# Performance work log

Hardware: AMD Instinct MI355X
Metric: run time of the kernel (lower is better)

## Reference

```python
import jax, jax.numpy as jnp
import numpy as np

D_MODEL = 256
NUM_HEADS = 4
D_HEAD = D_MODEL // NUM_HEADS
LN_EPS = 1e-5
NEG_INF = -1e9


def setup_inputs() -> dict:
    key = jax.random.key(0)
    ks = jax.random.split(key, 8)
    B, N = 4, 2048
    s = 1.0 / np.sqrt(D_MODEL)
    return {
        "x": jax.random.normal(ks[0], (B, N, D_MODEL), dtype=jnp.float32),
        "Wq": jax.random.normal(ks[1], (D_MODEL, D_MODEL), dtype=jnp.float32) * s,
        "Wk": jax.random.normal(ks[2], (D_MODEL, D_MODEL), dtype=jnp.float32) * s,
        "Wv": jax.random.normal(ks[3], (D_MODEL, D_MODEL), dtype=jnp.float32) * s,
        "Wo": jax.random.normal(ks[4], (D_MODEL, D_MODEL), dtype=jnp.float32) * s,
        "bo": jnp.zeros((D_MODEL,), dtype=jnp.float32),
        "gamma": jnp.ones((D_MODEL,), dtype=jnp.float32),
        "beta": jnp.zeros((D_MODEL,), dtype=jnp.float32),
        "k_neighbors": 8,
    }


def build_knn_adj(x, k):
    # x: [B, N, D]; returns symmetric 0/1 adjacency [B, N, N]
    B, N, _ = x.shape
    xn = x / jnp.maximum(jnp.linalg.norm(x, axis=-1, keepdims=True), 1e-12)
    sim = jnp.einsum('bnd,bmd->bnm', xn, xn)  # [B, N, N]
    _, idx = jax.lax.top_k(sim, k + 1)        # [B, N, k+1]
    b = jnp.arange(B)[:, None, None]
    r = jnp.arange(N)[None, :, None]
    adj = jnp.zeros((B, N, N), dtype=jnp.float32).at[b, r, idx].add(1.0)
    adj = jnp.maximum(adj, jnp.swapaxes(adj, 1, 2))
    return adj


def layer_norm(x, gamma, beta):
    mu = jnp.mean(x, axis=-1, keepdims=True)
    var = jnp.mean(jnp.square(x - mu), axis=-1, keepdims=True)
    return (x - mu) * jax.lax.rsqrt(var + LN_EPS) * gamma + beta


def reference(x, Wq, Wk, Wv, Wo, bo, gamma, beta, k_neighbors):
    B, N, D = x.shape
    adj = build_knn_adj(x, k_neighbors)  # [B, N, N]

    def split_heads(t):  # [B, N, D] -> [B, H, N, d]
        return jnp.transpose(t.reshape(B, N, NUM_HEADS, D_HEAD), (0, 2, 1, 3))

    q = split_heads(x @ Wq)
    k = split_heads(x @ Wk)
    v = split_heads(x @ Wv)

    scores = jnp.einsum('bhnd,bhmd->bhnm', q, k) / jnp.sqrt(jnp.float32(D_HEAD))
    scores = jnp.where(adj[:, None, :, :] > 0, scores, NEG_INF)
    attn = jax.nn.softmax(scores, axis=-1)  # dropout is identity at inference
    out = jnp.einsum('bhnm,bhmd->bhnd', attn, v)
    out = jnp.transpose(out, (0, 2, 1, 3)).reshape(B, N, D)
    out = out @ Wo + bo
    return layer_norm(x + out, gamma, beta)
```

## Files before the change

### kernel.cpp

```cpp
#include <hip/hip_runtime.h>
#include <hip/hip_bf16.h>
#include <math.h>

#define BATCH 4
#define N 2048
#define D 256
#define NH 4
#define DH 64
#define TOPK 9
#define NEG_BIG -1e30f

typedef __bf16 bf16;
typedef __bf16 bf16x4 __attribute__((ext_vector_type(4)));
typedef __bf16 bf16x8 __attribute__((ext_vector_type(8)));
typedef float f32x4 __attribute__((ext_vector_type(4)));

#define PK3(a,b,c) ((a) | ((b) << 2) | ((c) << 4))
#define PK6(a,b,c,d,e,f) ((a) | ((b) << 2) | ((c) << 4) | ((d) << 6) | ((e) << 8) | ((f) << 10))

#define WAITVM(Nc) __builtin_amdgcn_s_waitcnt((((Nc) & 0xf)) | (7u << 4) | (0xfu << 8) | ((((unsigned)(Nc)) >> 4) << 14))

__device__ __forceinline__ void async_cp16(const bf16* g, const bf16* l) {
  __builtin_amdgcn_global_load_lds(
      (const __attribute__((address_space(1))) void*)(uintptr_t)g,
      (__attribute__((address_space(3))) void*)(uintptr_t)l, 16, 0, 0);
}

__global__ __launch_bounds__(64) void prep_kernel(const float* __restrict__ x,
                                                  const float* __restrict__ Wq,
                                                  const float* __restrict__ Wk,
                                                  const float* __restrict__ Wv,
                                                  const float* __restrict__ Wo,
                                                  bf16* __restrict__ XsN,
                                                  bf16* __restrict__ Wt,
                                                  float* __restrict__ norms,
                                                  uint4* __restrict__ mask4) {
  int blk = blockIdx.x;
  int lane = threadIdx.x;
  if (blk < 8192) {
    float4 v = *(const float4*)(x + (size_t)blk * D + lane * 4);
    float ss = v.x * v.x + v.y * v.y + v.z * v.z + v.w * v.w;
    for (int off = 32; off; off >>= 1) ss += __shfl_down(ss, off);
    ss = __shfl(ss, 0);
    float nrm = fmaxf(sqrtf(ss), 1e-12f);
    if (lane == 0) norms[blk] = nrm;
    float sc = 1.0f / nrm;
    float xs[4] = {v.x * sc, v.y * sc, v.z * sc, v.w * sc};
    bf16* o = XsN + (size_t)blk * 512 + lane * 4;
#pragma unroll
    for (int j = 0; j < 4; ++j) {
      float xv = xs[j];
      bf16 h = (bf16)xv;
      o[j] = h;
      o[256 + j] = (bf16)(xv - (float)h);
    }
  } else if (blk < 9216) {
    int jj = blk - 8192;
    const float* W = (jj < 256) ? Wq : (jj < 512) ? Wk : (jj < 768) ? Wv : Wo;
    int j = jj & 255;
    bf16* dst = Wt + (size_t)jj * 512;
    for (int k = lane; k < 256; k += 64) {
      float w = W[(size_t)k * D + j];
      bf16 h = (bf16)w;
      dst[k] = h;
      dst[256 + k] = (bf16)(w - (float)h);
    }
  } else {
    int base = (blk - 9216) * 1024 + lane;
#pragma unroll
    for (int t = 0; t < 16; ++t)
      mask4[base + t * 64] = make_uint4(0, 0, 0, 0);
  }
}

__device__ __forceinline__ void gemm_core128x256(bf16* As, bf16* Bs,
                                                 const bf16* __restrict__ Ab,
                                                 const bf16* __restrict__ Bb,
                                                 void* __restrict__ Cvoid,
                                                 int ldc, int nsteps,
                                                 int amap, int bmap,
                                                 int row0, int col0,
                                                 int outmode, bool mirror,
                                                 const float* __restrict__ rowscale) {
  int tid = threadIdx.x;
  int lane = tid & 63;
  int wv = tid >> 6;
  int wm = (wv >> 1) * 64;
  int wn = (wv & 1) * 128;
  int fr = lane & 15;
  int G = lane >> 4;

  f32x4 acc[4][8] = {};

  auto issue = [&](int st, int buf) {
    int ch = st >> 3;
    int aoff = (((amap >> (ch * 2)) & 3) << 8) | ((st & 7) << 5);
    int boff = (((bmap >> (ch * 2)) & 3) << 8) | ((st & 7) << 5);
#pragma unroll
    for (int q = 0; q < 2; ++q) {
      int s = q * 256 + tid;
      int r = s >> 2, sl = s & 3;
      async_cp16(Ab + (size_t)r * 512 + ((sl ^ ((r >> 1) & 3)) << 3) + aoff,
                 &As[buf * 4096 + s * 8]);
    }
#pragma unroll
    for (int q = 0; q < 4; ++q) {
      int s = q * 256 + tid;
      int r = s >> 2, sl = s & 3;
      async_cp16(Bb + (size_t)r * 512 + ((sl ^ ((r >> 1) & 3)) << 3) + boff,
                 &Bs[buf * 8192 + s * 8]);
    }
  };

  issue(0, 0);
  for (int st = 0; st < nsteps; ++st) {
    int buf = st & 1;
    if (st + 1 < nsteps) {
      issue(st + 1, buf ^ 1);
      WAITVM(6);
    } else {
      WAITVM(0);
    }
    __builtin_amdgcn_s_barrier();
    bf16x8 af[4], bfr[8];
#pragma unroll
    for (int mi = 0; mi < 4; ++mi) {
      int r = wm + mi * 16 + fr;
      af[mi] = *(const bf16x8*)&As[buf * 4096 + r * 32 + ((G ^ ((r >> 1) & 3)) << 3)];
    }
#pragma unroll
    for (int nj = 0; nj < 8; ++nj) {
      int r = wn + nj * 16 + fr;
      bfr[nj] = *(const bf16x8*)&Bs[buf * 8192 + r * 32 + ((G ^ ((r >> 1) & 3)) << 3)];
    }
    __builtin_amdgcn_s_setprio(1);
#pragma unroll
    for (int mi = 0; mi < 4; ++mi)
#pragma unroll
      for (int nj = 0; nj < 8; ++nj)
        acc[mi][nj] = __builtin_amdgcn_mfma_f32_16x16x32_bf16(af[mi], bfr[nj], acc[mi][nj], 0, 0, 0);
    __builtin_amdgcn_s_setprio(0);
    __builtin_amdgcn_s_barrier();
  }

  int er = (lane >> 4) * 4;
  int ec = lane & 15;
#pragma unroll
  for (int mi = 0; mi < 4; ++mi) {
    int rb = row0 + wm + mi * 16 + er;
    float scl[4] = {1.f, 1.f, 1.f, 1.f};
    if (rowscale) {
      float4 s4 = *(const float4*)(rowscale + rb);
      scl[0] = s4.x; scl[1] = s4.y; scl[2] = s4.z; scl[3] = s4.w;
    }
#pragma unroll
    for (int nj = 0; nj < 8; ++nj) {
      int cb = col0 + wn + nj * 16 + ec;
      if (outmode == 1) {
        float* Cb = (float*)Cvoid;
#pragma unroll
        for (int reg = 0; reg < 4; ++reg)
          __builtin_nontemporal_store(acc[mi][nj][reg],
                                      &Cb[(size_t)(rb + reg) * ldc + cb]);
        if (mirror) {
          __builtin_nontemporal_store(acc[mi][nj],
                                      (f32x4*)&Cb[(size_t)cb * ldc + rb]);
        }
      } else {
        bf16* Cb = (bf16*)Cvoid;
#pragma unroll
        for (int reg = 0; reg < 4; ++reg)
          Cb[(size_t)(rb + reg) * ldc + cb] = (bf16)(acc[mi][nj][reg] * scl[reg]);
      }
    }
  }
}

__global__ __launch_bounds__(256, 2) void gemm_fused128x256_kernel(
    const bf16* __restrict__ XsN, float* __restrict__ sim,
    int amap_s, int bmap_s,
    const bf16* __restrict__ Wt, bf16* __restrict__ qkv,
    int amap_q, int bmap_q, const float* __restrict__ norms) {
  __shared__ bf16 As[2 * 128 * 32];
  __shared__ bf16 Bs[2 * 256 * 32];
  int g = blockIdx.x;
  if (g < 288) {
    int xcd = g & 7;
    int z = xcd >> 1;
    int t = (xcd & 1) * 36 + (g >> 3);
    int half = t & 1;
    int u = t >> 1;
    int by = 0;
    while (u >= 8 - by) { u -= 8 - by; ++by; }
    int bx = by + u;
    int row0 = by * 256 + half * 128;
    int col0 = bx * 256;
    gemm_core128x256(As, Bs,
                     XsN + (size_t)z * N * 512 + (size_t)row0 * 512,
                     XsN + (size_t)z * N * 512 + (size_t)col0 * 512,
                     sim + (size_t)z * N * N,
                     N, 24, amap_s, bmap_s, row0, col0,
                     1, bx != by, nullptr);
  } else {
    int t = g - 288;
    int xcd = t & 7;
    int slot = t >> 3;
    int z = xcd >> 1;
    int by = z * 16 + (xcd & 1) * 8 + slot / 3;
    int bx = slot % 3;
    gemm_core128x256(As, Bs,
                     XsN + (size_t)by * 128 * 512,
                     Wt + (size_t)bx * 256 * 512,
                     qkv, 768, 16, amap_q, bmap_q,
                     by * 128, bx * 256, 2, false, norms);
  }
}

__device__ __forceinline__ void gemm_core(bf16* As, bf16* Bs,
                                          const bf16* __restrict__ Ab,
                                          const bf16* __restrict__ Bb,
                                          void* __restrict__ Cvoid,
                                          int lda, int ldb, int ldc,
                                          int nsteps, int amap, int bmap,
                                          int row0, int col0,
                                          int outmode, bool mirror,
                                          const float* __restrict__ rowscale) {
  int tid = threadIdx.x;
  int lane = tid & 63;
  int wv = tid >> 6;
  int wm = (wv >> 1) * 64;
  int wn = (wv & 1) * 64;

  int rbase = tid >> 2;
  int gperm = (tid & 3) ^ ((rbase >> 1) & 3);
  const bf16* ga0 = Ab + (size_t)rbase * lda + gperm * 8;
  const bf16* gb0 = Bb + (size_t)rbase * ldb + gperm * 8;
  int ldsoff = tid * 8;

  int fr = lane & 15;
  int G = lane >> 4;

  f32x4 acc[4][4] = {};

  auto issue = [&](int st, int buf) {
    int ch = st >> 3;
    int aoff = (((amap >> (ch * 2)) & 3) << 8) | ((st & 7) << 5);
    int boff = (((bmap >> (ch * 2)) & 3) << 8) | ((st & 7) << 5);
#pragma unroll
    for (int q = 0; q < 2; ++q)
      async_cp16(ga0 + (size_t)q * 64 * lda + aoff, &As[buf * 4096 + ldsoff + q * 2048]);
#pragma unroll
    for (int q = 0; q < 2; ++q)
      async_cp16(gb0 + (size_t)q * 64 * ldb + boff, &Bs[buf * 4096 + ldsoff + q * 2048]);
  };

  issue(0, 0);
  for (int st = 0; st < nsteps; ++st) {
    int buf = st & 1;
    if (st + 1 < nsteps) {
      issue(st + 1, buf ^ 1);
      WAITVM(4);
    } else {
      WAITVM(0);
    }
    __builtin_amdgcn_s_barrier();
    bf16x8 af[4], bfr[4];
#pragma unroll
    for (int mi = 0; mi < 4; ++mi) {
      int r = wm + mi * 16 + fr;
      af[mi] = *(const bf16x8*)&As[buf * 4096 + r * 32 + ((G ^ ((r >> 1) & 3)) << 3)];
    }
#pragma unroll
    for (int nj = 0; nj < 4; ++nj) {
      int r = wn + nj * 16 + fr;
      bfr[nj] = *(const bf16x8*)&Bs[buf * 4096 + r * 32 + ((G ^ ((r >> 1) & 3)) << 3)];
    }
#pragma unroll
    for (int mi = 0; mi < 4; ++mi)
#pragma unroll
      for (int nj = 0; nj < 4; ++nj)
        acc[mi][nj] = __builtin_amdgcn_mfma_f32_16x16x32_bf16(af[mi], bfr[nj], acc[mi][nj], 0, 0, 0);
    __builtin_amdgcn_s_barrier();
  }

  int er = (lane >> 4) * 4;
  int ec = lane & 15;
#pragma unroll
  for (int mi = 0; mi < 4; ++mi) {
    int rb = row0 + wm + mi * 16 + er;
    float scl[4] = {1.f, 1.f, 1.f, 1.f};
    if (rowscale) {
      float4 s4 = *(const float4*)(rowscale + rb);
      scl[0] = s4.x; scl[1] = s4.y; scl[2] = s4.z; scl[3] = s4.w;
    }
#pragma unroll
    for (int nj = 0; nj < 4; ++nj) {
      int cb = col0 + wn + nj * 16 + ec;
      if (outmode == 1) {
        float* Cb = (float*)Cvoid;
#pragma unroll
        for (int reg = 0; reg < 4; ++reg)
          __builtin_nontemporal_store(acc[mi][nj][reg],
                                      &Cb[(size_t)(rb + reg) * ldc + cb]);
        if (mirror) {
#pragma unroll
          for (int reg = 0; reg < 4; ++reg)
            __builtin_nontemporal_store(acc[mi][nj][reg],
                                        &Cb[(size_t)cb * ldc + rb + reg]);
        }
      } else {
        bf16* Cb = (bf16*)Cvoid;
#pragma unroll
        for (int reg = 0; reg < 4; ++reg)
          Cb[(size_t)(rb + reg) * ldc + cb] = (bf16)(acc[mi][nj][reg] * scl[reg]);
      }
    }
  }
}

__global__ __launch_bounds__(256, 4) void gemm_sim_kernel(const bf16* __restrict__ XsN,
                                                          float* __restrict__ sim,
                                                          int amap, int bmap) {
  __shared__ bf16 As[2 * 128 * 32];
  __shared__ bf16 Bs[2 * 128 * 32];
  int g = blockIdx.x;
  int xcd = g & 7;
  int slot = g >> 3;
  int z = xcd >> 1;
  int t = (xcd & 1) * 68 + slot;
  int by = 0;
  while (t >= 16 - by) { t -= 16 - by; ++by; }
  int bx = by + t;
  gemm_core(As, Bs,
            XsN + (size_t)z * N * 512 + (size_t)by * 128 * 512,
            XsN + (size_t)z * N * 512 + (size_t)bx * 128 * 512,
            sim + (size_t)z * N * N,
            512, 512, N, 24, amap, bmap, by * 128, bx * 128,
            1, bx != by, nullptr);
}

__global__ __launch_bounds__(256, 4) void gemm_qkv_kernel(const bf16* __restrict__ XsN,
                                                          const bf16* __restrict__ Wt,
                                                          bf16* __restrict__ qkv,
                                                          int amap, int bmap,
                                                          const float* __restrict__ norms) {
  __shared__ bf16 As[2 * 128 * 32];
  __shared__ bf16 Bs[2 * 128 * 32];
  gemm_core(As, Bs,
            XsN + (size_t)blockIdx.y * 128 * 512,
            Wt + (size_t)blockIdx.x * 128 * 512,
            qkv, 512, 512, 768, 16, amap, bmap,
            blockIdx.y * 128, blockIdx.x * 128, 2, false, norms);
}

__global__ __launch_bounds__(64) void topk_adj_kernel(const float* __restrict__ sim,
                                                      unsigned* __restrict__ mask) {
  int row = blockIdx.x;
  int lane = threadIdx.x;
  int b = row >> 11, r = row & 2047;
  const float* srow = sim + (size_t)row * N;
  float v[32];
#pragma unroll
  for (int it = 0; it < 8; ++it) {
    float4 q = *(const float4*)(srow + it * 256 + lane * 4);
    v[it * 4 + 0] = q.x; v[it * 4 + 1] = q.y;
    v[it * 4 + 2] = q.z; v[it * 4 + 3] = q.w;
  }
  unsigned removed = 0;
  for (int rs = 0; rs < TOPK; ++rs) {
    float m = -3e38f;
    int mi = 0;
#pragma unroll
    for (int i = 0; i < 32; ++i) {
      float vv = ((removed >> i) & 1u) ? -3e38f : v[i];
      if (vv > m) { m = vv; mi = i; }
    }
    int gidx = ((mi >> 2) << 8) + lane * 4 + (mi & 3);
    for (int off = 32; off; off >>= 1) {
      float om = __shfl_down(m, off);
      int og = __shfl_down(gidx, off);
      if (om > m || (om == m && og < gidx)) { m = om; gidx = og; }
    }
    gidx = __shfl(gidx, 0);
    if (((gidx >> 2) & 63) == lane)
      removed |= 1u << (((gidx >> 8) << 2) | (gidx & 3));
    if (lane == 0) {
      atomicOr(&mask[(size_t)row * 64 + (gidx >> 5)], 1u << (gidx & 31));
      atomicOr(&mask[(((size_t)b << 11) + gidx) * 64 + (r >> 5)], 1u << (r & 31));
    }
  }
}

__global__ __launch_bounds__(256) void attn_kernel(const bf16* __restrict__ qkv,
                                                   const unsigned* __restrict__ mask,
                                                   bf16* __restrict__ aos) {
  __shared__ float sq[4][256];
  __shared__ unsigned short nbr[4][2048];
  __shared__ int s_nn[4];
  int wv = threadIdx.x >> 6;
  int lane = threadIdx.x & 63;
  int hl = lane >> 4;
  int g = blockIdx.x;
  int xcd = g & 7;
  int b = xcd >> 1;
  int tile = (xcd & 1) * 256 + (g >> 3);
  int bn = b * N + tile * 4 + wv;
  if (lane == 0) s_nn[wv] = 0;
  {
    bf16x4 qv = *(const bf16x4*)(qkv + (size_t)bn * 768 + lane * 4);
#pragma unroll
    for (int j = 0; j < 4; ++j) sq[wv][lane * 4 + j] = (float)qv[j];
  }
  __syncthreads();
  unsigned bits = mask[(size_t)bn * (N / 32) + lane];
  while (bits) {
    int bit = __ffs(bits) - 1;
    bits &= bits - 1;
    int p = atomicAdd(&s_nn[wv], 1);
    nbr[wv][p] = (unsigned short)(lane * 32 + bit);
  }
  __syncthreads();
  int nn = s_nn[wv];
  const bf16* base = qkv + (size_t)b * N * 768;
  float acc2[4] = {0.f, 0.f, 0.f, 0.f};

  auto score4 = [&](int j, float* s) {
    const bf16* kr = base + (size_t)j * 768 + 256;
#pragma unroll
    for (int h = 0; h < 4; ++h) {
      float a = 0.f;
#pragma unroll
      for (int c = 0; c < DH; c += 8) {
        bf16x8 kk = *(const bf16x8*)(kr + h * DH + c);
#pragma unroll
        for (int t = 0; t < 8; ++t) a += sq[wv][h * DH + c + t] * (float)kk[t];
      }
      s[h] = a * 0.125f;
    }
  };

  if (nn <= 64) {
    float s[4] = {NEG_BIG, NEG_BIG, NEG_BIG, NEG_BIG};
    if (lane < nn) score4(nbr[wv][lane], s);
    float w[4], l[4];
#pragma unroll
    for (int h = 0; h < 4; ++h) {
      float m = s[h];
      for (int off = 32; off; off >>= 1) m = fmaxf(m, __shfl_down(m, off));
      m = __shfl(m, 0);
      float e = (lane < nn) ? __expf(s[h] - m) : 0.f;
      float ls = e;
      for (int off = 32; off; off >>= 1) ls += __shfl_down(ls, off);
      l[h] = __shfl(ls, 0);
      w[h] = e;
    }
    auto pickw = [&](int ii) {
      float a0 = __shfl(w[0], ii), a1 = __shfl(w[1], ii);
      float a2 = __shfl(w[2], ii), a3 = __shfl(w[3], ii);
      return hl == 0 ? a0 : (hl == 1 ? a1 : (hl == 2 ? a2 : a3));
    };
    int i = 0;
    for (; i + 4 <= nn; i += 4) {
      int j0 = nbr[wv][i + 0], j1 = nbr[wv][i + 1];
      int j2 = nbr[wv][i + 2], j3 = nbr[wv][i + 3];
      bf16x4 v0 = *(const bf16x4*)(base + (size_t)j0 * 768 + 512 + lane * 4);
      bf16x4 v1 = *(const bf16x4*)(base + (size_t)j1 * 768 + 512 + lane * 4);
      bf16x4 v2 = *(const bf16x4*)(base + (size_t)j2 * 768 + 512 + lane * 4);
      bf16x4 v3 = *(const bf16x4*)(base + (size_t)j3 * 768 + 512 + lane * 4);
      float w0 = pickw(i + 0), w1 = pickw(i + 1);
      float w2 = pickw(i + 2), w3 = pickw(i + 3);
#pragma unroll
      for (int t = 0; t < 4; ++t)
        acc2[t] += w0 * (float)v0[t] + w1 * (float)v1[t] +
                   w2 * (float)v2[t] + w3 * (float)v3[t];
    }
    for (; i < nn; ++i) {
      bf16x4 v0 = *(const bf16x4*)(base + (size_t)nbr[wv][i] * 768 + 512 + lane * 4);
      float w0 = pickw(i);
#pragma unroll
      for (int t = 0; t < 4; ++t) acc2[t] += w0 * (float)v0[t];
    }
    float ldiv = hl == 0 ? l[0] : (hl == 1 ? l[1] : (hl == 2 ? l[2] : l[3]));
#pragma unroll
    for (int t = 0; t < 4; ++t) acc2[t] /= ldiv;
  } else {
    float m[4] = {NEG_BIG, NEG_BIG, NEG_BIG, NEG_BIG};
    for (int i0 = 0; i0 < nn; i0 += 64) {
      float s[4] = {NEG_BIG, NEG_BIG, NEG_BIG, NEG_BIG};
      if (i0 + lane < nn) score4(nbr[wv][i0 + lane], s);
#pragma unroll
      for (int h = 0; h < 4; ++h) m[h] = fmaxf(m[h], s[h]);
    }
#pragma unroll
    for (int h = 0; h < 4; ++h) {
      for (int off = 32; off; off >>= 1) m[h] = fmaxf(m[h], __shfl_down(m[h], off));
      m[h] = __shfl(m[h], 0);
    }
    float l[4] = {0.f, 0.f, 0.f, 0.f};
    for (int i0 = 0; i0 < nn; i0 += 64) {
      float s[4] = {NEG_BIG, NEG_BIG, NEG_BIG, NEG_BIG};
      if (i0 + lane < nn) score4(nbr[wv][i0 + lane], s);
      float e[4];
#pragma unroll
      for (int h = 0; h < 4; ++h) {
        e[h] = (i0 + lane < nn) ? __expf(s[h] - m[h]) : 0.f;
        float ls = e[h];
        for (int off = 32; off; off >>= 1) ls += __shfl_down(ls, off);
        l[h] += __shfl(ls, 0);
      }
      auto picke = [&](int ii) {
        float a0 = __shfl(e[0], ii), a1 = __shfl(e[1], ii);
        float a2 = __shfl(e[2], ii), a3 = __shfl(e[3], ii);
        return hl == 0 ? a0 : (hl == 1 ? a1 : (hl == 2 ? a2 : a3));
      };
      int lim = min(64, nn - i0);
      for (int ii = 0; ii < lim; ++ii) {
        bf16x4 v0 = *(const bf16x4*)(base + (size_t)nbr[wv][i0 + ii] * 768 + 512 + lane * 4);
        float w0 = picke(ii);
#pragma unroll
        for (int t = 0; t < 4; ++t) acc2[t] += w0 * (float)v0[t];
      }
    }
    float ldiv = hl == 0 ? l[0] : (hl == 1 ? l[1] : (hl == 2 ? l[2] : l[3]));
#pragma unroll
    for (int t = 0; t < 4; ++t) acc2[t] /= ldiv;
  }
  bf16x4 hi4, lo4;
#pragma unroll
  for (int t = 0; t < 4; ++t) {
    float a = acc2[t];
    bf16 h8 = (bf16)a;
    hi4[t] = h8;
    lo4[t] = (bf16)(a - (float)h8);
  }
  *(bf16x4*)(aos + (size_t)bn * 512 + lane * 4) = hi4;
  *(bf16x4*)(aos + (size_t)bn * 512 + 256 + lane * 4) = lo4;
}

__global__ __launch_bounds__(256) void projln_kernel(const bf16* __restrict__ A,
                                                     const bf16* __restrict__ Bw,
                                                     const float* __restrict__ x,
                                                     const float* __restrict__ bo,
                                                     const float* __restrict__ gamma,
                                                     const float* __restrict__ beta,
                                                     float* __restrict__ out) {
  __shared__ bf16 As[2 * 32 * 32];
  __shared__ bf16 Bs[2 * 256 * 32];
  __shared__ float rsum[32][4];
  __shared__ float rsq[32][4];
  int tid = threadIdx.x;
  int lane = tid & 63;
  int wv = tid >> 6;
  int wn = wv * 64;
  int row0 = blockIdx.x * 32;

  int rt = tid >> 2;
  int ra = tid >> 2;
  int gpa = (tid & 3) ^ ((ra >> 1) & 3);
  const bf16* ga0 = A + (size_t)(row0 + ra) * 512 + gpa * 8;

  int fr = lane & 15;
  int G = lane >> 4;

  f32x4 acc[2][4] = {};

  auto issue = [&](int st, int buf) {
    int aoff = ((st >> 3) << 8) | ((st & 7) << 5);
    int boff = (st & 7) << 5;
    if (tid < 128)
      async_cp16(ga0 + aoff, &As[buf * 1024 + tid * 8]);
#pragma unroll
    for (int q = 0; q < 4; ++q) {
      int rb = q * 64 + rt;
      int gpb = (tid & 3) ^ ((rb >> 1) & 3);
      async_cp16(Bw + (size_t)rb * 512 + gpb * 8 + boff,
                 &Bs[buf * 8192 + (q * 256 + tid) * 8]);
    }
  };

  issue(0, 0);
  for (int st = 0; st < 16; ++st) {
    int buf = st & 1;
    if (st + 1 < 16) {
      issue(st + 1, buf ^ 1);
      WAITVM(4);
    } else {
      WAITVM(0);
    }
    __builtin_amdgcn_s_barrier();
    bf16x8 af[2], bfr[4];
#pragma unroll
    for (int mi = 0; mi < 2; ++mi) {
      int r = mi * 16 + fr;
      af[mi] = *(const bf16x8*)&As[buf * 1024 + r * 32 + ((G ^ ((r >> 1) & 3)) << 3)];
    }
#pragma unroll
    for (int nj = 0; nj < 4; ++nj) {
      int r = wn + nj * 16 + fr;
      bfr[nj] = *(const bf16x8*)&Bs[buf * 8192 + r * 32 + ((G ^ ((r >> 1) & 3)) << 3)];
    }
#pragma unroll
    for (int mi = 0; mi < 2; ++mi)
#pragma unroll
      for (int nj = 0; nj < 4; ++nj)
        acc[mi][nj] = __builtin_amdgcn_mfma_f32_16x16x32_bf16(af[mi], bfr[nj], acc[mi][nj], 0, 0, 0);
    __builtin_amdgcn_s_barrier();
  }

  int er = (lane >> 4) * 4;
  int ec = lane & 15;
  float bo_c[4], ga_c[4], be_c[4];
#pragma unroll
  for (int nj = 0; nj < 4; ++nj) {
    int c = wn + nj * 16 + ec;
    bo_c[nj] = bo[c]; ga_c[nj] = gamma[c]; be_c[nj] = beta[c];
  }
#pragma unroll
  for (int mi = 0; mi < 2; ++mi)
#pragma unroll
    for (int reg = 0; reg < 4; ++reg) {
      int rloc = mi * 16 + er + reg;
      const float* xr = x + (size_t)(row0 + rloc) * D;
      float su = 0.f, s2 = 0.f;
#pragma unroll
      for (int nj = 0; nj < 4; ++nj) {
        float u = acc[mi][nj][reg] + bo_c[nj] + xr[wn + nj * 16 + ec];
        su += u; s2 += u * u;
      }
#pragma unroll
      for (int m = 1; m <= 8; m <<= 1) {
        su += __shfl_xor(su, m);
        s2 += __shfl_xor(s2, m);
      }
      if (ec == 0) { rsum[rloc][wv] = su; rsq[rloc][wv] = s2; }
    }
  __syncthreads();
#pragma unroll
  for (int mi = 0; mi < 2; ++mi)
#pragma unroll
    for (int reg = 0; reg < 4; ++reg) {
      int rloc = mi * 16 + er + reg;
      float s = rsum[rloc][0] + rsum[rloc][1] + rsum[rloc][2] + rsum[rloc][3];
      float q2 = rsq[rloc][0] + rsq[rloc][1] + rsq[rloc][2] + rsq[rloc][3];
      float mean = s * (1.0f / D);
      float var = q2 * (1.0f / D) - mean * mean;
      float rstd = rsqrtf(var + 1e-5f);
      const float* xr = x + (size_t)(row0 + rloc) * D;
      float* orow = out + (size_t)(row0 + rloc) * D;
#pragma unroll
      for (int nj = 0; nj < 4; ++nj) {
        float u = acc[mi][nj][reg] + bo_c[nj] + xr[wn + nj * 16 + ec];
        orow[wn + nj * 16 + ec] = (u - mean) * rstd * ga_c[nj] + be_c[nj];
      }
    }
}

extern "C" void kernel_launch(void* const* d_in, const int* in_sizes, int n_in,
                              void* d_out, int out_size, void* d_ws, size_t ws_size,
                              hipStream_t stream) {
  const float* x     = (const float*)d_in[0];
  const float* Wq    = (const float*)d_in[1];
  const float* Wk    = (const float*)d_in[2];
  const float* Wv    = (const float*)d_in[3];
  const float* Wo    = (const float*)d_in[4];
  const float* bo    = (const float*)d_in[5];
  const float* gamma = (const float*)d_in[6];
  const float* beta  = (const float*)d_in[7];
  float* out = (float*)d_out;

  char* ws = (char*)d_ws;
  bf16* XsN      = (bf16*)(ws);
  float* sim     = (float*)(ws + 12582912);
  float* norms   = (float*)(ws + 79691776);
  unsigned* mask = (unsigned*)(ws + 79986688);
  bf16* Wt       = (bf16*)(ws + 82083840);

  bool big = ws_size >= (size_t)125000000;
  bf16* qkv = (bf16*)(ws + (big ? 83132416 : 12582912));
  bf16* aos = (bf16*)(ws + (big ? 95715328 : 37748736));

  const int AMAP_SIM = PK6(0, 0, 1, 0, 0, 0);
  const int BMAP_SIM = PK6(0, 1, 0, 0, 0, 0);
  const int AMAP_2T  = PK3(0, 1, 0);
  const int BMAP_2T  = PK3(0, 0, 1);

  prep_kernel<<<9344, 64, 0, stream>>>(x, Wq, Wk, Wv, Wo, XsN, Wt, norms,
                                       (uint4*)mask);

  if (big) {
    gemm_fused128x256_kernel<<<480, 256, 0, stream>>>(
        XsN, sim, AMAP_SIM, BMAP_SIM, Wt, qkv, AMAP_2T, BMAP_2T, norms);
    topk_adj_kernel<<<BATCH * N, 64, 0, stream>>>(sim, mask);
  } else {
    gemm_sim_kernel<<<544, 256, 0, stream>>>(XsN, sim, AMAP_SIM, BMAP_SIM);
    topk_adj_kernel<<<BATCH * N, 64, 0, stream>>>(sim, mask);
    gemm_qkv_kernel<<<dim3(6, 64), 256, 0, stream>>>(XsN, Wt, qkv,
                                                     AMAP_2T, BMAP_2T, norms);
  }

  attn_kernel<<<(BATCH * N) / 4, 256, 0, stream>>>(qkv, mask, aos);

  projln_kernel<<<256, 256, 0, stream>>>(aos, Wt + (size_t)768 * 512,
                                         x, bo, gamma, beta, out);
}
```

Measured before the change: 189.5 us.

## Tile weight transpose via LDS, interleave fused GEMM blocks, two rows per topk wave

The weight transpose/split in prep now uses 64x64 LDS tiles with coalesced float4 reads and vectorized bf16x8 writes instead of strided per-column reads. The fused sim/QKV GEMM interleaves sim and QKV blocks (3:2 pattern) across the grid rather than running all sim blocks first, to balance work over time. The top-k kernel processes two rows per wave with four waves per block, giving more independent work per wave to hide shuffle latency. These add register pressure in top-k and shared memory in prep.

Result: slower. 193.7 us (+2.2%).

```diff
diff --git a/kernel.cpp b/kernel.cpp
--- a/kernel.cpp
+++ b/kernel.cpp
@@ -35,6 +35,7 @@
                                                   bf16* __restrict__ Wt,
                                                   float* __restrict__ norms,
                                                   uint4* __restrict__ mask4) {
+  __shared__ float T[64][65];
   int blk = blockIdx.x;
   int lane = threadIdx.x;
   if (blk < 8192) {
@@ -54,19 +55,41 @@
       o[j] = h;
       o[256 + j] = (bf16)(xv - (float)h);
     }
-  } else if (blk < 9216) {
-    int jj = blk - 8192;
-    const float* W = (jj < 256) ? Wq : (jj < 512) ? Wk : (jj < 768) ? Wv : Wo;
-    int j = jj & 255;
-    bf16* dst = Wt + (size_t)jj * 512;
-    for (int k = lane; k < 256; k += 64) {
-      float w = W[(size_t)k * D + j];
-      bf16 h = (bf16)w;
-      dst[k] = h;
-      dst[256 + k] = (bf16)(w - (float)h);
+  } else if (blk < 8256) {
+    int tj = blk - 8192;
+    int wsel = tj >> 4;
+    int tile = tj & 15;
+    int tr = (tile >> 2) * 64;
+    int tc = (tile & 3) * 64;
+    const float* W = (wsel == 0) ? Wq : (wsel == 1) ? Wk : (wsel == 2) ? Wv : Wo;
+    int l4 = lane & 15, lr = lane >> 4;
+#pragma unroll
+    for (int it = 0; it < 16; ++it) {
+      int k = tr + it * 4 + lr;
+      float4 w4 = *(const float4*)(W + (size_t)k * D + tc + l4 * 4);
+      T[l4 * 4 + 0][it * 4 + lr] = w4.x;
+      T[l4 * 4 + 1][it * 4 + lr] = w4.y;
+      T[l4 * 4 + 2][it * 4 + lr] = w4.z;
+      T[l4 * 4 + 3][it * 4 + lr] = w4.w;
+    }
+    __syncthreads();
+    int jj = wsel * 256 + tc + lane;
+    bf16* dst = Wt + (size_t)jj * 512 + tr;
+#pragma unroll
+    for (int c = 0; c < 8; ++c) {
+      bf16x8 hv, mv;
+#pragma unroll
+      for (int t = 0; t < 8; ++t) {
+        float w = T[lane][c * 8 + t];
+        bf16 h = (bf16)w;
+        hv[t] = h;
+        mv[t] = (bf16)(w - (float)h);
+      }
+      *(bf16x8*)(dst + c * 8) = hv;
+      *(bf16x8*)(dst + 256 + c * 8) = mv;
     }
   } else {
-    int base = (blk - 9216) * 1024 + lane;
+    int base = (blk - 8256) * 1024 + lane;
 #pragma unroll
     for (int t = 0; t < 16; ++t)
       mask4[base + t * 64] = make_uint4(0, 0, 0, 0);
@@ -184,15 +207,17 @@
   __shared__ bf16 As[2 * 128 * 32];
   __shared__ bf16 Bs[2 * 256 * 32];
   int g = blockIdx.x;
-  if (g < 288) {
-    int xcd = g & 7;
+  int rr = g % 5, u = g / 5;
+  if (rr == 0 || rr == 1 || rr == 3) {
+    int s = u * 3 + (rr == 3 ? 2 : rr);
+    int xcd = s & 7;
     int z = xcd >> 1;
-    int t = (xcd & 1) * 36 + (g >> 3);
+    int t = (xcd & 1) * 36 + (s >> 3);
     int half = t & 1;
-    int u = t >> 1;
+    int uu = t >> 1;
     int by = 0;
-    while (u >= 8 - by) { u -= 8 - by; ++by; }
-    int bx = by + u;
+    while (uu >= 8 - by) { uu -= 8 - by; ++by; }
+    int bx = by + uu;
     int row0 = by * 256 + half * 128;
     int col0 = bx * 256;
     gemm_core128x256(As, Bs,
@@ -202,9 +227,9 @@
                      N, 24, amap_s, bmap_s, row0, col0,
                      1, bx != by, nullptr);
   } else {
-    int t = g - 288;
-    int xcd = t & 7;
-    int slot = t >> 3;
+    int q = u * 2 + (rr == 4 ? 1 : 0);
+    int xcd = q & 7;
+    int slot = q >> 3;
     int z = xcd >> 1;
     int by = z * 16 + (xcd & 1) * 8 + slot / 3;
     int bx = slot % 3;
@@ -353,40 +378,55 @@
             blockIdx.y * 128, blockIdx.x * 128, 2, false, norms);
 }
 
-__global__ __launch_bounds__(64) void topk_adj_kernel(const float* __restrict__ sim,
-                                                      unsigned* __restrict__ mask) {
-  int row = blockIdx.x;
-  int lane = threadIdx.x;
-  int b = row >> 11, r = row & 2047;
-  const float* srow = sim + (size_t)row * N;
-  float v[32];
+__global__ __launch_bounds__(256) void topk_adj_kernel(const float* __restrict__ sim,
+                                                       unsigned* __restrict__ mask) {
+  int wv = threadIdx.x >> 6;
+  int lane = threadIdx.x & 63;
+  int pr = blockIdx.x * 4 + wv;
+  int r0 = pr * 2, r1 = r0 + 1;
+  int b = r0 >> 11;
+  const float* s0 = sim + (size_t)r0 * N;
+  const float* s1 = sim + (size_t)r1 * N;
+  float va[32], vb[32];
 #pragma unroll
   for (int it = 0; it < 8; ++it) {
-    float4 q = *(const float4*)(srow + it * 256 + lane * 4);
-    v[it * 4 + 0] = q.x; v[it * 4 + 1] = q.y;
-    v[it * 4 + 2] = q.z; v[it * 4 + 3] = q.w;
-  }
-  unsigned removed = 0;
+    float4 qa = *(const float4*)(s0 + it * 256 + lane * 4);
+    float4 qb = *(const float4*)(s1 + it * 256 + lane * 4);
+    va[it * 4 + 0] = qa.x; va[it * 4 + 1] = qa.y;
+    va[it * 4 + 2] = qa.z; va[it * 4 + 3] = qa.w;
+    vb[it * 4 + 0] = qb.x; vb[it * 4 + 1] = qb.y;
+    vb[it * 4 + 2] = qb.z; vb[it * 4 + 3] = qb.w;
+  }
+  unsigned rma = 0, rmb = 0;
   for (int rs = 0; rs < TOPK; ++rs) {
-    float m = -3e38f;
-    int mi = 0;
+    float ma = -3e38f, mb = -3e38f;
+    int ia = 0, ib = 0;
 #pragma unroll
     for (int i = 0; i < 32; ++i) {
-      float vv = ((removed >> i) & 1u) ? -3e38f : v[i];
-      if (vv > m) { m = vv; mi = i; }
-    }
-    int gidx = ((mi >> 2) << 8) + lane * 4 + (mi & 3);
+      float xa = ((rma >> i) & 1u) ? -3e38f : va[i];
+      if (xa > ma) { ma = xa; ia = i; }
+      float xb = ((rmb >> i) & 1u) ? -3e38f : vb[i];
+      if (xb > mb) { mb = xb; ib = i; }
+    }
+    int ga = ((ia >> 2) << 8) + lane * 4 + (ia & 3);
+    int gb = ((ib >> 2) << 8) + lane * 4 + (ib & 3);
     for (int off = 32; off; off >>= 1) {
-      float om = __shfl_down(m, off);
-      int og = __shfl_down(gidx, off);
-      if (om > m || (om == m && og < gidx)) { m = om; gidx = og; }
-    }
-    gidx = __shfl(gidx, 0);
-    if (((gidx >> 2) & 63) == lane)
-      removed |= 1u << (((gidx >> 8) << 2) | (gidx & 3));
+      float oa = __shfl_down(ma, off);
+      int og = __shfl_down(ga, off);
+      float ob = __shfl_down(mb, off);
+      int oh = __shfl_down(gb, off);
+      if (oa > ma || (oa == ma && og < ga)) { ma = oa; ga = og; }
+      if (ob > mb || (ob == mb && oh < gb)) { mb = ob; gb = oh; }
+    }
+    ga = __shfl(ga, 0);
+    gb = __shfl(gb, 0);
+    if (((ga >> 2) & 63) == lane) rma |= 1u << (((ga >> 8) << 2) | (ga & 3));
+    if (((gb >> 2) & 63) == lane) rmb |= 1u << (((gb >> 8) << 2) | (gb & 3));
     if (lane == 0) {
-      atomicOr(&mask[(size_t)row * 64 + (gidx >> 5)], 1u << (gidx & 31));
-      atomicOr(&mask[(((size_t)b << 11) + gidx) * 64 + (r >> 5)], 1u << (r & 31));
+      atomicOr(&mask[(size_t)r0 * 64 + (ga >> 5)], 1u << (ga & 31));
+      atomicOr(&mask[(((size_t)b << 11) + ga) * 64 + ((r0 & 2047) >> 5)], 1u << ((r0 & 2047) & 31));
+      atomicOr(&mask[(size_t)r1 * 64 + (gb >> 5)], 1u << (gb & 31));
+      atomicOr(&mask[(((size_t)b << 11) + gb) * 64 + ((r1 & 2047) >> 5)], 1u << ((r1 & 2047) & 31));
     }
   }
 }
@@ -684,16 +724,16 @@
   const int AMAP_2T  = PK3(0, 1, 0);
   const int BMAP_2T  = PK3(0, 0, 1);
 
-  prep_kernel<<<9344, 64, 0, stream>>>(x, Wq, Wk, Wv, Wo, XsN, Wt, norms,
+  prep_kernel<<<8384, 64, 0, stream>>>(x, Wq, Wk, Wv, Wo, XsN, Wt, norms,
                                        (uint4*)mask);
 
   if (big) {
     gemm_fused128x256_kernel<<<480, 256, 0, stream>>>(
         XsN, sim, AMAP_SIM, BMAP_SIM, Wt, qkv, AMAP_2T, BMAP_2T, norms);
-    topk_adj_kernel<<<BATCH * N, 64, 0, stream>>>(sim, mask);
+    topk_adj_kernel<<<1024, 256, 0, stream>>>(sim, mask);
   } else {
     gemm_sim_kernel<<<544, 256, 0, stream>>>(XsN, sim, AMAP_SIM, BMAP_SIM);
-    topk_adj_kernel<<<BATCH * N, 64, 0, stream>>>(sim, mask);
+    topk_adj_kernel<<<1024, 256, 0, stream>>>(sim, mask);
     gemm_qkv_kernel<<<dim3(6, 64), 256, 0, stream>>>(XsN, Wt, qkv,
                                                      AMAP_2T, BMAP_2T, norms);
   }
```
